# Optimization experiments

Measured on AMD Instinct MI355X. Metric: run time of the kernel, lower is better.

## Reference

```python
import jax, jax.numpy as jnp
import numpy as np

B, N, C, H, SR = 4, 4096, 512, 8, 2
HD = C // H           # head_dim = 64
SCALE = HD ** -0.5
EPS = 1e-5


def setup_inputs() -> dict:
    key = jax.random.key(0)
    ks = jax.random.split(key, 6)
    s = 0.02
    return {
        "x": jax.random.normal(ks[0], (B, N, C), jnp.float32),
        # weights stored [in, out] (transposed vs torch nn.Linear)
        "w_qkv": jax.random.normal(ks[1], (C, 3 * C), jnp.float32) * s,
        "w_proj": jax.random.normal(ks[2], (C, C), jnp.float32) * s,
        "b_proj": jnp.zeros((C,), jnp.float32),
        # depthwise conv: OIHW with I=1, feature_group_count=C
        "w_sr_conv": jax.random.normal(ks[3], (C, 1, SR, SR), jnp.float32) * s,
        "b_sr_conv": jnp.zeros((C,), jnp.float32),
        "sr_norm_scale": jnp.ones((C,), jnp.float32),
        "sr_norm_bias": jnp.zeros((C,), jnp.float32),
        "w_sr_linear": jax.random.normal(ks[4], (C, HD), jnp.float32) * s,
        "b_sr_linear": jnp.zeros((HD,), jnp.float32),
    }


def reference(x, w_qkv, w_proj, b_proj, w_sr_conv, b_sr_conv,
              sr_norm_scale, sr_norm_bias, w_sr_linear, b_sr_linear):
    Bx, Nx, Cx = x.shape
    # qkv projection (no bias), split into heads
    qkv = (x @ w_qkv).reshape(Bx, Nx, 3, H, HD).transpose(2, 0, 3, 1, 4)  # [3,B,H,N,HD]
    q, k, v = qkv[0], qkv[1], qkv[2]

    # spatial-reduction branch (sr_ratio > 1)
    S = int(Nx ** 0.5)
    x_ = x.transpose(0, 2, 1).reshape(Bx, Cx, S, S)
    x_ = jax.lax.conv_general_dilated(
        x_, w_sr_conv, window_strides=(SR, SR), padding='VALID',
        dimension_numbers=('NCHW', 'OIHW', 'NCHW'), feature_group_count=Cx)
    x_ = x_ + b_sr_conv[None, :, None, None]
    x_ = x_.reshape(Bx, Cx, -1).transpose(0, 2, 1)  # [B, M, C], M = (S/SR)^2
    # LayerNorm over C
    mu = jnp.mean(x_, axis=-1, keepdims=True)
    var = jnp.var(x_, axis=-1, keepdims=True)
    x_ = (x_ - mu) * jax.lax.rsqrt(var + EPS) * sr_norm_scale + sr_norm_bias
    x_ = x_ @ w_sr_linear + b_sr_linear  # [B, M, HD]

    # K/V compression: softmax-weighted pooling of k and v by x_ scores
    scores_k = jax.nn.softmax(jnp.einsum('bmd,bhnd->bhmn', x_, k), axis=-1)
    k = jnp.einsum('bhmn,bhnd->bhmd', scores_k, k)  # [B,H,M,HD]
    scores_v = jax.nn.softmax(jnp.einsum('bmd,bhnd->bhmn', x_, v), axis=-1)
    v = jnp.einsum('bhmn,bhnd->bhmd', scores_v, v)  # [B,H,M,HD]

    # standard attention against compressed K/V
    attn = jax.nn.softmax(jnp.einsum('bhnd,bhmd->bhnm', q, k) * SCALE, axis=-1)
    out = jnp.einsum('bhnm,bhmd->bhnd', attn, v)        # [B,H,N,HD]
    out = out.transpose(0, 2, 1, 3).reshape(Bx, Nx, Cx)  # [B,N,C]
    return out @ w_proj + b_proj
```

## Files before the change

### kernel.cpp

```cpp
#include <hip/hip_runtime.h>

typedef float f32x4 __attribute__((ext_vector_type(4)));
typedef short bf16x8 __attribute__((ext_vector_type(8)));
typedef _Float16 f16x8 __attribute__((ext_vector_type(8)));
typedef __fp16 fp16x2 __attribute__((ext_vector_type(2)));

constexpr int kB  = 4;
constexpr int kN  = 4096;
constexpr int kC  = 512;
constexpr int kH  = 8;
constexpr int kHD = 64;
constexpr int kM  = 1024;
constexpr int kC3 = 1536;

__device__ inline unsigned pkh(float a, float b) {
    union { fp16x2 h; unsigned u; } u;
    u.h = __builtin_amdgcn_cvt_pkrtz(a, b);
    return u.u;
}

__device__ inline float fdot2a(unsigned ph, unsigned ones, float acc) {
    asm("v_dot2_f32_f16 %0, %1, %2, %0" : "+v"(acc) : "v"(ph), "v"(ones));
    return acc;
}

__device__ inline void swap32p(unsigned &a, unsigned &b) {
#if __has_builtin(__builtin_amdgcn_permlane32_swap)
    auto r = __builtin_amdgcn_permlane32_swap(a, b, false, false);
    a = r[0]; b = r[1];
#else
    asm volatile("v_permlane32_swap_b32 %0, %1" : "+v"(a), "+v"(b));
#endif
}
__device__ inline void swap16p(unsigned &a, unsigned &b) {
#if __has_builtin(__builtin_amdgcn_permlane16_swap)
    auto r = __builtin_amdgcn_permlane16_swap(a, b, false, false);
    a = r[0]; b = r[1];
#else
    asm volatile("v_permlane16_swap_b32 %0, %1" : "+v"(a), "+v"(b));
#endif
}

__global__ __launch_bounds__(256) void cvt_f16(
    const float* __restrict__ X, _Float16* __restrict__ Y, int n4)
{
    int i = blockIdx.x * 256 + threadIdx.x;
    if (i >= n4) return;
    float4 v = ((const float4*)X)[i];
    union { _Float16 h[4]; short4 s; } u;
    u.h[0] = (_Float16)v.x; u.h[1] = (_Float16)v.y;
    u.h[2] = (_Float16)v.z; u.h[3] = (_Float16)v.w;
    ((short4*)Y)[i] = u.s;
}

__global__ __launch_bounds__(256) void wcvtT16(
    const float* __restrict__ W, int K, int N, _Float16* __restrict__ T16)
{
    __shared__ float T[64][65];
    const int n0 = blockIdx.x * 64, k0 = blockIdx.y * 64;
    const int t = threadIdx.x;
#pragma unroll
    for (int i = 0; i < 4; i++) {
        int c = t + i * 256;
        int row = c >> 4, col4 = (c & 15) * 4;
        *(float4*)&T[row][col4] = *(const float4*)&W[(size_t)(k0 + row) * N + n0 + col4];
    }
    __syncthreads();
#pragma unroll
    for (int i = 0; i < 4; i++) {
        int c = t + i * 256;
        int nrow = c >> 4, kc4 = (c & 15) * 4;
        union { _Float16 h[4]; short4 s; } u;
        u.h[0] = (_Float16)T[kc4 + 0][nrow];
        u.h[1] = (_Float16)T[kc4 + 1][nrow];
        u.h[2] = (_Float16)T[kc4 + 2][nrow];
        u.h[3] = (_Float16)T[kc4 + 3][nrow];
        *(short4*)&T16[(size_t)(n0 + nrow) * K + k0 + kc4] = u.s;
    }
}

__global__ __launch_bounds__(256) void transpose_hd(
    const short* __restrict__ s0, const short* __restrict__ s1,
    short* __restrict__ d0, short* __restrict__ d1, int nTok)
{
    __shared__ short T[64][72];
    const short* src = blockIdx.z == 0 ? s0 : s1;
    short*       dst = blockIdx.z == 0 ? d0 : d1;
    const int n0 = blockIdx.x * 64, bh = blockIdx.y;
    const int t = threadIdx.x;
#pragma unroll
    for (int i = 0; i < 2; i++) {
        int c = t + i * 256;
        int row = c >> 3, j = (c & 7) * 8;
        *(bf16x8*)&T[row][j] = *(const bf16x8*)&src[((size_t)bh * nTok + n0 + row) * 64 + j];
    }
    __syncthreads();
#pragma unroll
    for (int i = 0; i < 2; i++) {
        int c = t + i * 256;
        int drow = c >> 3, j = (c & 7) * 8;
        bf16x8 v;
#pragma unroll
        for (int q = 0; q < 8; q++) v[q] = T[j + q][drow];
        *(bf16x8*)&dst[((size_t)bh * 64 + drow) * nTok + n0 + j] = v;
    }
}

__global__ __launch_bounds__(256) void gemm_f16(
    const _Float16* __restrict__ A, const _Float16* __restrict__ B,
    int Md, int Nd, int Kd, int mode, float qscale,
    const float* __restrict__ bias, float* __restrict__ Cf,
    _Float16* __restrict__ q, _Float16* __restrict__ k, _Float16* __restrict__ v)
{
    __shared__ _Float16 Ash[128][40], Bsh[128][40];
    const int t = threadIdx.x, lane = t & 63, L = lane & 15, quad = lane >> 4;
    const int wave = t >> 6, wm = wave >> 1, wn = wave & 1;
    const int bm = blockIdx.y * 128, bn = blockIdx.x * 128;

    f32x4 acc[4][4];
#pragma unroll
    for (int i = 0; i < 4; i++)
#pragma unroll
        for (int j = 0; j < 4; j++) acc[i][j] = (f32x4){0.f, 0.f, 0.f, 0.f};

    for (int k0 = 0; k0 < Kd; k0 += 32) {
#pragma unroll
        for (int i = 0; i < 2; i++) {
            int c = t + i * 256;
            int row = c >> 2, j = (c & 3) * 8;
            *(f16x8*)&Ash[row][j] = *(const f16x8*)&A[(size_t)(bm + row) * Kd + k0 + j];
            *(f16x8*)&Bsh[row][j] = *(const f16x8*)&B[(size_t)(bn + row) * Kd + k0 + j];
        }
        __syncthreads();
        f16x8 af[4];
#pragma unroll
        for (int mi = 0; mi < 4; mi++)
            af[mi] = *(const f16x8*)&Ash[wm * 64 + mi * 16 + L][quad * 8];
#pragma unroll
        for (int ni = 0; ni < 4; ni++) {
            f16x8 bf = *(const f16x8*)&Bsh[wn * 64 + ni * 16 + L][quad * 8];
#pragma unroll
            for (int mi = 0; mi < 4; mi++)
                acc[mi][ni] = __builtin_amdgcn_mfma_f32_16x16x32_f16(af[mi], bf, acc[mi][ni], 0, 0, 0);
        }
        __syncthreads();
    }

    if (mode == 0) {
#pragma unroll
        for (int ni = 0; ni < 4; ni++) {
            int col = bn + wn * 64 + ni * 16 + L;
            float bb = bias ? bias[col] : 0.f;
#pragma unroll
            for (int mi = 0; mi < 4; mi++)
#pragma unroll
                for (int r = 0; r < 4; r++) {
                    int row = bm + wm * 64 + mi * 16 + quad * 4 + r;
                    Cf[(size_t)row * Nd + col] = acc[mi][ni][r] + bb;
                }
        }
    } else {
#pragma unroll
        for (int ni = 0; ni < 4; ni++) {
            int col = bn + wn * 64 + ni * 16 + L;
            int s = col >> 9, h = (col >> 6) & 7, d = col & 63;
            _Float16* dst = s == 0 ? q : s == 1 ? k : v;
            float sc = (s == 0) ? qscale : 1.0f;
#pragma unroll
            for (int mi = 0; mi < 4; mi++)
#pragma unroll
                for (int r = 0; r < 4; r++) {
                    int row = bm + wm * 64 + mi * 16 + quad * 4 + r;
                    int b = row >> 12, n = row & 4095;
                    size_t idx = (((size_t)b * 8 + h) * 4096 + n) * 64 + d;
                    dst[idx] = (_Float16)(acc[mi][ni][r] * sc);
                }
        }
    }
}

__global__ __launch_bounds__(256) void sr_fused(
    const float* __restrict__ x, const float* __restrict__ wconv,
    const float* __restrict__ bconv, const float* __restrict__ gamma,
    const float* __restrict__ beta, const float* __restrict__ wlin,
    const float* __restrict__ blin, _Float16* __restrict__ xsr)
{
    __shared__ float nbuf[512];
    __shared__ float red[8];
    __shared__ float stats[2];
    __shared__ float pbuf[4][64];

    const int m = blockIdx.x, b = blockIdx.y;
    const int oy = m >> 5, ox = m & 31;
    const int t = threadIdx.x;
    const float* xb = x + (size_t)b * kN * kC;

    float vals[2], s = 0.f, sq = 0.f;
#pragma unroll
    for (int i = 0; i < 2; i++) {
        int c = t + i * 256;
        float acc = bconv[c];
#pragma unroll
        for (int dy = 0; dy < 2; dy++)
#pragma unroll
            for (int dx = 0; dx < 2; dx++) {
                int n = (oy * 2 + dy) * 64 + (ox * 2 + dx);
                acc += xb[(size_t)n * kC + c] * wconv[c * 4 + dy * 2 + dx];
            }
        vals[i] = acc;
        s += acc; sq += acc * acc;
    }
#pragma unroll
    for (int off = 32; off > 0; off >>= 1) {
        s  += __shfl_down(s,  off);
        sq += __shfl_down(sq, off);
    }
    if ((t & 63) == 0) { red[t >> 6] = s; red[4 + (t >> 6)] = sq; }
    __syncthreads();
    if (t == 0) {
        float ts = red[0] + red[1] + red[2] + red[3];
        float tq = red[4] + red[5] + red[6] + red[7];
        float mean = ts * (1.f / 512.f);
        float var  = tq * (1.f / 512.f) - mean * mean;
        stats[0] = mean;
        stats[1] = rsqrtf(var + 1e-5f);
    }
    __syncthreads();
    const float mean = stats[0], rstd = stats[1];
#pragma unroll
    for (int i = 0; i < 2; i++) {
        int c = t + i * 256;
        nbuf[c] = (vals[i] - mean) * rstd * gamma[c] + beta[c];
    }
    __syncthreads();
    const int d = t & 63, part = t >> 6;
    float p = 0.f;
    for (int c = part * 128; c < (part + 1) * 128; c++)
        p += nbuf[c] * wlin[c * 64 + d];
    pbuf[part][d] = p;
    __syncthreads();
    if (t < 64) {
        float o = pbuf[0][t] + pbuf[1][t] + pbuf[2][t] + pbuf[3][t] + blin[t];
        xsr[((size_t)b * kM + m) * kHD + t] = (_Float16)(o * 1.44269504089f);
    }
}

__global__ __launch_bounds__(256, 4) void flash_mfma(
    const _Float16* __restrict__ Q, long q_bs, long q_hs,
    const _Float16* __restrict__ K0, const _Float16* __restrict__ K1,
    long k_bs, long k_hs,
    const _Float16* __restrict__ VT0, const _Float16* __restrict__ VT1,
    long v_bs, long v_hs, int v_rs,
    _Float16* __restrict__ O,
    long o_bs, long o_hs, long o_rs, int o_cs,
    int nKtot, int nChunks, int kvMerge,
    float* __restrict__ Opart, float* __restrict__ MLpart)
{
    __shared__ _Float16 Ks[2][64][72];
    __shared__ _Float16 VTs[2][64][72];
    const int t = threadIdx.x, lane = t & 63, L = lane & 15, quad = lane >> 4;
    const int wave = t >> 6;
    const int h = blockIdx.x & 7;
    const int rest = (blockIdx.x >> 3) + (gridDim.x >> 3) * blockIdx.y;
    int b, which, nB;
    if (kvMerge) { b = blockIdx.z >> 1; which = blockIdx.z & 1; nB = gridDim.z >> 1; }
    else         { b = blockIdx.z;      which = 0;              nB = gridDim.z; }
    const int nMblk = gridDim.x / nChunks;
    const int mblk = rest / nChunks, chunk = rest % nChunks;
    const int m0 = mblk * 128;
    const int nkc = nKtot / nChunks, nbeg = chunk * nkc, nend = nbeg + nkc;
    const unsigned kOnes = 0x3C003C00u;

    const _Float16* K_ = (which ? K1 : K0) + (size_t)b * k_bs + (size_t)h * k_hs;
    const _Float16* V_ = (which ? VT1 : VT0) + (size_t)b * v_bs + (size_t)h * v_hs;

    f16x8 qf[2][2];
#pragma unroll
    for (int s = 0; s < 2; s++) {
        const size_t qrow = (size_t)b * q_bs + (size_t)h * q_hs
                          + (size_t)(m0 + wave * 32 + s * 16 + L) * 64;
        qf[s][0] = *(const f16x8*)&Q[qrow + quad * 8];
        qf[s][1] = *(const f16x8*)&Q[qrow + 32 + quad * 8];
    }

    f32x4 Oacc[2][4];
#pragma unroll
    for (int s = 0; s < 2; s++)
#pragma unroll
        for (int i = 0; i < 4; i++) Oacc[s][i] = (f32x4){0.f, 0.f, 0.f, 0.f};
    float li[2] = {0.f, 0.f};

    const int sr = t >> 3, sj = (t & 7) * 8;

    {
        f16x8 a0 = *(const f16x8*)&K_[(size_t)(nbeg + sr) * 64 + sj];
        f16x8 a1 = *(const f16x8*)&K_[(size_t)(nbeg + sr + 32) * 64 + sj];
        f16x8 a2 = *(const f16x8*)&V_[(size_t)sr * v_rs + nbeg + sj];
        f16x8 a3 = *(const f16x8*)&V_[(size_t)(sr + 32) * v_rs + nbeg + sj];
        *(f16x8*)&Ks[0][sr][sj]       = a0;
        *(f16x8*)&Ks[0][sr + 32][sj]  = a1;
        *(f16x8*)&VTs[0][sr][sj]      = a2;
        *(f16x8*)&VTs[0][sr + 32][sj] = a3;
    }
    __syncthreads();

    int cur = 0;
    for (int n0 = nbeg; n0 < nend; n0 += 64) {
        int nn = (n0 + 64 < nend) ? n0 + 64 : nbeg;
        f16x8 kp0 = *(const f16x8*)&K_[(size_t)(nn + sr) * 64 + sj];
        f16x8 kp1 = *(const f16x8*)&K_[(size_t)(nn + sr + 32) * 64 + sj];
        f16x8 vp0 = *(const f16x8*)&V_[(size_t)sr * v_rs + nn + sj];
        f16x8 vp1 = *(const f16x8*)&V_[(size_t)(sr + 32) * v_rs + nn + sj];

        unsigned d0[2][4], d1[2][4];
#pragma unroll
        for (int c = 0; c < 4; c++) {
            f16x8 k0 = *(const f16x8*)&Ks[cur][c * 16 + L][quad * 8];
            f16x8 k1 = *(const f16x8*)&Ks[cur][c * 16 + L][32 + quad * 8];
#pragma unroll
            for (int s = 0; s < 2; s++) {
                f32x4 a = (f32x4){0.f, 0.f, 0.f, 0.f};
                a = __builtin_amdgcn_mfma_f32_16x16x32_f16(k0, qf[s][0], a, 0, 0, 0);
                a = __builtin_amdgcn_mfma_f32_16x16x32_f16(k1, qf[s][1], a, 0, 0, 0);
                float p0 = exp2f(a[0]);
                float p1 = exp2f(a[1]);
                float p2 = exp2f(a[2]);
                float p3 = exp2f(a[3]);
                d0[s][c] = pkh(p0, p1);
                d1[s][c] = pkh(p2, p3);
                li[s] = fdot2a(d0[s][c], kOnes, li[s]);
                li[s] = fdot2a(d1[s][c], kOnes, li[s]);
            }
        }

        f16x8 pt[2][2];
#pragma unroll
        for (int s = 0; s < 2; s++)
#pragma unroll
            for (int h2 = 0; h2 < 2; h2++) {
                unsigned a0 = d0[s][h2 * 2], b0 = d0[s][h2 * 2 + 1];
                swap32p(a0, b0); swap16p(a0, b0);
                unsigned a1 = d1[s][h2 * 2], b1 = d1[s][h2 * 2 + 1];
                swap32p(a1, b1); swap16p(a1, b1);
                union { unsigned u[4]; f16x8 v; } U;
                U.u[0] = a0; U.u[1] = a1; U.u[2] = b0; U.u[3] = b1;
                pt[s][h2] = U.v;
            }

#pragma unroll
        for (int h2 = 0; h2 < 2; h2++) {
#pragma unroll
            for (int dch = 0; dch < 4; dch++) {
                f16x8 vt = *(const f16x8*)&VTs[cur][dch * 16 + L][h2 * 32 + quad * 8];
                Oacc[0][dch] = __builtin_amdgcn_mfma_f32_16x16x32_f16(vt, pt[0][h2], Oacc[0][dch], 0, 0, 0);
                Oacc[1][dch] = __builtin_amdgcn_mfma_f32_16x16x32_f16(vt, pt[1][h2], Oacc[1][dch], 0, 0, 0);
            }
        }

        *(f16x8*)&Ks[cur ^ 1][sr][sj]       = kp0;
        *(f16x8*)&Ks[cur ^ 1][sr + 32][sj]  = kp1;
        *(f16x8*)&VTs[cur ^ 1][sr][sj]      = vp0;
        *(f16x8*)&VTs[cur ^ 1][sr + 32][sj] = vp1;
        __syncthreads();
        cur ^= 1;
    }

    float lt[2];
#pragma unroll
    for (int s = 0; s < 2; s++) {
        float v = li[s];
        v += __shfl_xor(v, 16);
        v += __shfl_xor(v, 32);
        lt[s] = v;
    }

    if (Opart) {
        int pid = (((which * nB + b) * gridDim.y + h) * nMblk + mblk) * nChunks + chunk;
        float* Ob = Opart + (size_t)pid * (128 * 64);
        float* Mb = MLpart + (size_t)pid * 256;
#pragma unroll
        for (int s = 0; s < 2; s++) {
            int mloc = wave * 32 + s * 16 + L;
#pragma unroll
            for (int dch = 0; dch < 4; dch++)
                *(f32x4*)&Ob[mloc * 64 + dch * 16 + quad * 4] = Oacc[s][dch];
            if (quad == 0) { Mb[mloc] = 0.f; Mb[128 + mloc] = lt[s]; }
        }
    } else {
#pragma unroll
        for (int s = 0; s < 2; s++) {
            float inv = 1.f / lt[s];
            size_t base = (size_t)b * o_bs + (size_t)h * o_hs
                        + (size_t)(m0 + wave * 32 + s * 16 + L) * o_rs;
#pragma unroll
            for (int dch = 0; dch < 4; dch++)
#pragma unroll
                for (int r = 0; r < 4; r++) {
                    int d = dch * 16 + quad * 4 + r;
                    O[base + (size_t)d * o_cs] = (_Float16)(Oacc[s][dch][r] * inv);
                }
        }
    }
}

__global__ __launch_bounds__(256) void flash_combine(
    const float* __restrict__ Opart, const float* __restrict__ MLpart,
    int nMblk, int nChunks, float cl2,
    _Float16* __restrict__ O, long o_bs, long o_hs, long o_rs, int o_cs)
{
    const int t = threadIdx.x;
    const int b = blockIdx.z, h = blockIdx.y;
    const int qm = blockIdx.x * 4 + (t >> 6), d = t & 63;
    const int mblk = qm >> 7, qloc = qm & 127;
    const int pb = ((b * gridDim.y + h) * nMblk + mblk) * nChunks;
    float mf = -INFINITY;
    for (int c = 0; c < nChunks; c++)
        mf = fmaxf(mf, MLpart[(size_t)(pb + c) * 256 + qloc]);
    float num = 0.f, den = 0.f;
    for (int c = 0; c < nChunks; c++) {
        float mc = MLpart[(size_t)(pb + c) * 256 + qloc];
        float lc = MLpart[(size_t)(pb + c) * 256 + 128 + qloc];
        float w = exp2f((mc - mf) * cl2);
        den += lc * w;
        num += Opart[(size_t)(pb + c) * 8192 + qloc * 64 + d] * w;
    }
    size_t addr = (size_t)b * o_bs + (size_t)h * o_hs + (size_t)qm * o_rs + (size_t)d * o_cs;
    O[addr] = (_Float16)(num / den);
}

extern "C" void kernel_launch(void* const* d_in, const int* in_sizes, int n_in,
                              void* d_out, int out_size, void* d_ws, size_t ws_size,
                              hipStream_t stream)
{
    const float* x      = (const float*)d_in[0];
    const float* w_qkv  = (const float*)d_in[1];
    const float* w_proj = (const float*)d_in[2];
    const float* b_proj = (const float*)d_in[3];
    const float* w_conv = (const float*)d_in[4];
    const float* b_conv = (const float*)d_in[5];
    const float* g_ln   = (const float*)d_in[6];
    const float* b_ln   = (const float*)d_in[7];
    const float* w_lin  = (const float*)d_in[8];
    const float* b_lin  = (const float*)d_in[9];
    float* out = (float*)d_out;
    (void)in_sizes; (void)n_in; (void)out_size; (void)ws_size;

    short* p = (short*)d_ws;
    size_t off = 0;
    auto alloc = [&](size_t n) { short* r = p + off; off += n; return r; };

    const size_t TN = (size_t)kB * kH * kN * kHD;
    const size_t TM = (size_t)kB * kH * kM * kHD;

    _Float16* xf16 = (_Float16*)alloc((size_t)kB * kN * kC);
    _Float16* ao   = xf16;

    _Float16* wq16 = (_Float16*)alloc((size_t)kC3 * kC);
    _Float16* wp16 = (_Float16*)alloc((size_t)kC * kC);
    _Float16* qh  = (_Float16*)alloc(TN);
    _Float16* kh  = (_Float16*)alloc(TN);
    _Float16* vh  = (_Float16*)alloc(TN);
    _Float16* kT  = (_Float16*)alloc(TN);
    _Float16* vT  = (_Float16*)alloc(TN);
    _Float16* xsr = (_Float16*)alloc((size_t)kB * kM * kHD);
    _Float16* kc  = (_Float16*)alloc(TM);
    _Float16* vc  = (_Float16*)alloc(TM);
    _Float16* vcT = (_Float16*)alloc(TM);
    float* MLpart = (float*)alloc((size_t)2048 * 256 * 2);
    float* Opart  = (float*)alloc((size_t)2048 * 8192 * 2);

    const int NCH = 4;

    cvt_f16<<<(kB * kN * kC / 4 + 255) / 256, 256, 0, stream>>>(
        x, xf16, kB * kN * kC / 4);

    wcvtT16<<<dim3(kC3 / 64, kC / 64), 256, 0, stream>>>(w_qkv, kC, kC3, wq16);
    wcvtT16<<<dim3(kC / 64, kC / 64), 256, 0, stream>>>(w_proj, kC, kC, wp16);

    gemm_f16<<<dim3(kC3 / 128, kB * kN / 128), 256, 0, stream>>>(
        xf16, wq16, kB * kN, kC3, kC, 1, 0.18033688f, nullptr, nullptr,
        qh, kh, vh);

    transpose_hd<<<dim3(kN / 64, kB * kH, 2), 256, 0, stream>>>(
        (const short*)kh, (const short*)vh, (short*)kT, (short*)vT, kN);

    sr_fused<<<dim3(kM, kB), 256, 0, stream>>>(
        x, w_conv, b_conv, g_ln, b_ln, w_lin, b_lin, xsr);

    flash_mfma<<<dim3(8 * NCH, kH, kB * 2), 256, 0, stream>>>(
        xsr, (long)kM * kHD, 0L,
        kh, vh, (long)kH * kN * kHD, (long)kN * kHD,
        kT, vT, (long)kH * kHD * kN, (long)kHD * kN, kN,
        nullptr, 0L, 0L, 0L, 0,
        kN, NCH, 1, Opart, MLpart);
    flash_combine<<<dim3(kM / 4, kH, kB), 256, 0, stream>>>(
        Opart, MLpart, 8, NCH, 1.44269504089f,
        kc, (long)kH * kM * kHD, (long)kM * kHD, 64L, 1);
    flash_combine<<<dim3(kM / 4, kH, kB), 256, 0, stream>>>(
        Opart + (size_t)1024 * 8192, MLpart + (size_t)1024 * 256, 8, NCH,
        1.44269504089f,
        vc, (long)kH * kM * kHD, (long)kM * kHD, 64L, 1);
    transpose_hd<<<dim3(kM / 64, kB * kH, 1), 256, 0, stream>>>(
        (const short*)vc, (const short*)vc, (short*)vcT, (short*)vcT, kM);

    flash_mfma<<<dim3(32, kH, kB), 256, 0, stream>>>(
        qh, (long)kH * kN * kHD, (long)kN * kHD,
        kc, kc, (long)kH * kM * kHD, (long)kM * kHD,
        vcT, vcT, (long)kH * kHD * kM, (long)kHD * kM, kM,
        ao, (long)kN * kC, 64L, (long)kC, 1,
        kM, 1, 0, nullptr, nullptr);

    gemm_f16<<<dim3(kC / 128, kB * kN / 128), 256, 0, stream>>>(
        ao, wp16, kB * kN, kC, kC, 0, 1.0f, b_proj, out,
        nullptr, nullptr, nullptr);
}
```

Measured before the change: 409.1 us.

## Load K/V fragments directly from global memory instead of LDS double buffer

The flash attention kernel no longer stages K and V^T tiles through a double-buffered shared-memory array. Each wave now loads its MFMA operand fragments straight from global memory (relying on L1/L2 caching, since all four waves read the same tiles). This drops the LDS writes and reads and the full __syncthreads, keeping only a bare s_barrier. In exchange every wave issues redundant global loads, and the software prefetch that overlapped the next tile's load with compute is lost.

```diff
diff --git a/kernel.cpp b/kernel.cpp
--- a/kernel.cpp
+++ b/kernel.cpp
@@ -256,8 +256,6 @@
     int nKtot, int nChunks, int kvMerge,
     float* __restrict__ Opart, float* __restrict__ MLpart)
 {
-    __shared__ _Float16 Ks[2][64][72];
-    __shared__ _Float16 VTs[2][64][72];
     const int t = threadIdx.x, lane = t & 63, L = lane & 15, quad = lane >> 4;
     const int wave = t >> 6;
     const int h = blockIdx.x & 7;
@@ -274,6 +272,9 @@
     const _Float16* K_ = (which ? K1 : K0) + (size_t)b * k_bs + (size_t)h * k_hs;
     const _Float16* V_ = (which ? VT1 : VT0) + (size_t)b * v_bs + (size_t)h * v_hs;
 
+    const _Float16* Krow = K_ + (size_t)L * 64 + quad * 8;
+    const _Float16* Vrow = V_ + (size_t)L * v_rs + quad * 8;
+
     f16x8 qf[2][2];
 #pragma unroll
     for (int s = 0; s < 2; s++) {
@@ -290,38 +291,23 @@
         for (int i = 0; i < 4; i++) Oacc[s][i] = (f32x4){0.f, 0.f, 0.f, 0.f};
     float li[2] = {0.f, 0.f};
 
-    const int sr = t >> 3, sj = (t & 7) * 8;
-
-    {
-        f16x8 a0 = *(const f16x8*)&K_[(size_t)(nbeg + sr) * 64 + sj];
-        f16x8 a1 = *(const f16x8*)&K_[(size_t)(nbeg + sr + 32) * 64 + sj];
-        f16x8 a2 = *(const f16x8*)&V_[(size_t)sr * v_rs + nbeg + sj];
-        f16x8 a3 = *(const f16x8*)&V_[(size_t)(sr + 32) * v_rs + nbeg + sj];
-        *(f16x8*)&Ks[0][sr][sj]       = a0;
-        *(f16x8*)&Ks[0][sr + 32][sj]  = a1;
-        *(f16x8*)&VTs[0][sr][sj]      = a2;
-        *(f16x8*)&VTs[0][sr + 32][sj] = a3;
-    }
-    __syncthreads();
-
-    int cur = 0;
     for (int n0 = nbeg; n0 < nend; n0 += 64) {
-        int nn = (n0 + 64 < nend) ? n0 + 64 : nbeg;
-        f16x8 kp0 = *(const f16x8*)&K_[(size_t)(nn + sr) * 64 + sj];
-        f16x8 kp1 = *(const f16x8*)&K_[(size_t)(nn + sr + 32) * 64 + sj];
-        f16x8 vp0 = *(const f16x8*)&V_[(size_t)sr * v_rs + nn + sj];
-        f16x8 vp1 = *(const f16x8*)&V_[(size_t)(sr + 32) * v_rs + nn + sj];
+        f16x8 kf0[4], kf1[4];
+#pragma unroll
+        for (int c = 0; c < 4; c++) {
+            const _Float16* kr = Krow + (size_t)(n0 + c * 16) * 64;
+            kf0[c] = *(const f16x8*)kr;
+            kf1[c] = *(const f16x8*)(kr + 32);
+        }
 
         unsigned d0[2][4], d1[2][4];
 #pragma unroll
         for (int c = 0; c < 4; c++) {
-            f16x8 k0 = *(const f16x8*)&Ks[cur][c * 16 + L][quad * 8];
-            f16x8 k1 = *(const f16x8*)&Ks[cur][c * 16 + L][32 + quad * 8];
 #pragma unroll
             for (int s = 0; s < 2; s++) {
                 f32x4 a = (f32x4){0.f, 0.f, 0.f, 0.f};
-                a = __builtin_amdgcn_mfma_f32_16x16x32_f16(k0, qf[s][0], a, 0, 0, 0);
-                a = __builtin_amdgcn_mfma_f32_16x16x32_f16(k1, qf[s][1], a, 0, 0, 0);
+                a = __builtin_amdgcn_mfma_f32_16x16x32_f16(kf0[c], qf[s][0], a, 0, 0, 0);
+                a = __builtin_amdgcn_mfma_f32_16x16x32_f16(kf1[c], qf[s][1], a, 0, 0, 0);
                 float p0 = exp2f(a[0]);
                 float p1 = exp2f(a[1]);
                 float p2 = exp2f(a[2]);
@@ -333,6 +319,14 @@
             }
         }
 
+        f16x8 vf[2][4];
+#pragma unroll
+        for (int h2 = 0; h2 < 2; h2++)
+#pragma unroll
+            for (int dch = 0; dch < 4; dch++)
+                vf[h2][dch] = *(const f16x8*)(Vrow + (size_t)(dch * 16) * v_rs
+                                              + n0 + h2 * 32);
+
         f16x8 pt[2][2];
 #pragma unroll
         for (int s = 0; s < 2; s++)
@@ -351,18 +345,12 @@
         for (int h2 = 0; h2 < 2; h2++) {
 #pragma unroll
             for (int dch = 0; dch < 4; dch++) {
-                f16x8 vt = *(const f16x8*)&VTs[cur][dch * 16 + L][h2 * 32 + quad * 8];
-                Oacc[0][dch] = __builtin_amdgcn_mfma_f32_16x16x32_f16(vt, pt[0][h2], Oacc[0][dch], 0, 0, 0);
-                Oacc[1][dch] = __builtin_amdgcn_mfma_f32_16x16x32_f16(vt, pt[1][h2], Oacc[1][dch], 0, 0, 0);
+                Oacc[0][dch] = __builtin_amdgcn_mfma_f32_16x16x32_f16(vf[h2][dch], pt[0][h2], Oacc[0][dch], 0, 0, 0);
+                Oacc[1][dch] = __builtin_amdgcn_mfma_f32_16x16x32_f16(vf[h2][dch], pt[1][h2], Oacc[1][dch], 0, 0, 0);
             }
         }
 
-        *(f16x8*)&Ks[cur ^ 1][sr][sj]       = kp0;
-        *(f16x8*)&Ks[cur ^ 1][sr + 32][sj]  = kp1;
-        *(f16x8*)&VTs[cur ^ 1][sr][sj]      = vp0;
-        *(f16x8*)&VTs[cur ^ 1][sr + 32][sj] = vp1;
-        __syncthreads();
-        cur ^= 1;
+        __builtin_amdgcn_s_barrier();
     }
 
     float lt[2];
```

After: 612.1 us. 49.6% more time.

## Use direct global-to-LDS loads in GEMM and store flash partials in fp16

Applied to the files above, without the earlier changes.

The GEMM tile loads now use global_load_lds to write straight into unpadded shared memory, skipping the round trip through registers. The split-K flash partial outputs are normalized and stored as fp16 with only the row sums kept. The combine step then becomes a sum weighted by those row sums, with no max pass, which roughly halves partial-buffer traffic. The trade-offs are possible LDS bank conflicts from removing the padding and slightly lower precision in the stored partials. The simplified combine relies on the max already being zero, which the old code also assumed (it wrote 0 for the max).

```diff
diff --git a/kernel.cpp b/kernel.cpp
--- a/kernel.cpp
+++ b/kernel.cpp
@@ -39,6 +39,12 @@
 #else
     asm volatile("v_permlane16_swap_b32 %0, %1" : "+v"(a), "+v"(b));
 #endif
+}
+
+__device__ inline void gl_lds16(const _Float16* g, _Float16* l) {
+    __builtin_amdgcn_global_load_lds(
+        (const __attribute__((address_space(1))) unsigned int*)(const void*)g,
+        (__attribute__((address_space(3))) unsigned int*)(void*)l, 16, 0, 0);
 }
 
 __global__ __launch_bounds__(256) void cvt_f16(
@@ -112,10 +118,11 @@
     const float* __restrict__ bias, float* __restrict__ Cf,
     _Float16* __restrict__ q, _Float16* __restrict__ k, _Float16* __restrict__ v)
 {
-    __shared__ _Float16 Ash[128][40], Bsh[128][40];
+    __shared__ _Float16 Ash[128][32], Bsh[128][32];
     const int t = threadIdx.x, lane = t & 63, L = lane & 15, quad = lane >> 4;
     const int wave = t >> 6, wm = wave >> 1, wn = wave & 1;
     const int bm = blockIdx.y * 128, bn = blockIdx.x * 128;
+    const int r16 = lane >> 2, c16 = lane & 3;
 
     f32x4 acc[4][4];
 #pragma unroll
@@ -126,10 +133,10 @@
     for (int k0 = 0; k0 < Kd; k0 += 32) {
 #pragma unroll
         for (int i = 0; i < 2; i++) {
-            int c = t + i * 256;
-            int row = c >> 2, j = (c & 3) * 8;
-            *(f16x8*)&Ash[row][j] = *(const f16x8*)&A[(size_t)(bm + row) * Kd + k0 + j];
-            *(f16x8*)&Bsh[row][j] = *(const f16x8*)&B[(size_t)(bn + row) * Kd + k0 + j];
+            int chunk = wave * 2 + i;
+            int row = chunk * 16 + r16;
+            gl_lds16(&A[(size_t)(bm + row) * Kd + k0 + c16 * 8], &Ash[chunk * 16][0]);
+            gl_lds16(&B[(size_t)(bn + row) * Kd + k0 + c16 * 8], &Bsh[chunk * 16][0]);
         }
         __syncthreads();
         f16x8 af[4];
@@ -254,7 +261,7 @@
     _Float16* __restrict__ O,
     long o_bs, long o_hs, long o_rs, int o_cs,
     int nKtot, int nChunks, int kvMerge,
-    float* __restrict__ Opart, float* __restrict__ MLpart)
+    _Float16* __restrict__ Opart, float* __restrict__ MLpart)
 {
     __shared__ _Float16 Ks[2][64][72];
     __shared__ _Float16 VTs[2][64][72];
@@ -376,15 +383,21 @@
 
     if (Opart) {
         int pid = (((which * nB + b) * gridDim.y + h) * nMblk + mblk) * nChunks + chunk;
-        float* Ob = Opart + (size_t)pid * (128 * 64);
-        float* Mb = MLpart + (size_t)pid * 256;
+        _Float16* Ob = Opart + (size_t)pid * (128 * 64);
+        float* Mb = MLpart + (size_t)pid * 128;
 #pragma unroll
         for (int s = 0; s < 2; s++) {
             int mloc = wave * 32 + s * 16 + L;
-#pragma unroll
-            for (int dch = 0; dch < 4; dch++)
-                *(f32x4*)&Ob[mloc * 64 + dch * 16 + quad * 4] = Oacc[s][dch];
-            if (quad == 0) { Mb[mloc] = 0.f; Mb[128 + mloc] = lt[s]; }
+            float inv = 1.f / lt[s];
+#pragma unroll
+            for (int dch = 0; dch < 4; dch++) {
+                union { _Float16 h[4]; uint2 u; } U;
+#pragma unroll
+                for (int r = 0; r < 4; r++)
+                    U.h[r] = (_Float16)(Oacc[s][dch][r] * inv);
+                *(uint2*)&Ob[mloc * 64 + dch * 16 + quad * 4] = U.u;
+            }
+            if (quad == 0) Mb[mloc] = lt[s];
         }
     } else {
 #pragma unroll
@@ -404,8 +417,8 @@
 }
 
 __global__ __launch_bounds__(256) void flash_combine(
-    const float* __restrict__ Opart, const float* __restrict__ MLpart,
-    int nMblk, int nChunks, float cl2,
+    const _Float16* __restrict__ Opart, const float* __restrict__ MLpart,
+    int nMblk, int nChunks,
     _Float16* __restrict__ O, long o_bs, long o_hs, long o_rs, int o_cs)
 {
     const int t = threadIdx.x;
@@ -413,16 +426,11 @@
     const int qm = blockIdx.x * 4 + (t >> 6), d = t & 63;
     const int mblk = qm >> 7, qloc = qm & 127;
     const int pb = ((b * gridDim.y + h) * nMblk + mblk) * nChunks;
-    float mf = -INFINITY;
-    for (int c = 0; c < nChunks; c++)
-        mf = fmaxf(mf, MLpart[(size_t)(pb + c) * 256 + qloc]);
     float num = 0.f, den = 0.f;
     for (int c = 0; c < nChunks; c++) {
-        float mc = MLpart[(size_t)(pb + c) * 256 + qloc];
-        float lc = MLpart[(size_t)(pb + c) * 256 + 128 + qloc];
-        float w = exp2f((mc - mf) * cl2);
-        den += lc * w;
-        num += Opart[(size_t)(pb + c) * 8192 + qloc * 64 + d] * w;
+        float lc = MLpart[(size_t)(pb + c) * 128 + qloc];
+        num += lc * (float)Opart[(size_t)(pb + c) * 8192 + qloc * 64 + d];
+        den += lc;
     }
     size_t addr = (size_t)b * o_bs + (size_t)h * o_hs + (size_t)qm * o_rs + (size_t)d * o_cs;
     O[addr] = (_Float16)(num / den);
@@ -466,8 +474,8 @@
     _Float16* kc  = (_Float16*)alloc(TM);
     _Float16* vc  = (_Float16*)alloc(TM);
     _Float16* vcT = (_Float16*)alloc(TM);
-    float* MLpart = (float*)alloc((size_t)2048 * 256 * 2);
-    float* Opart  = (float*)alloc((size_t)2048 * 8192 * 2);
+    float*    MLpart = (float*)alloc((size_t)2048 * 128 * 2);
+    _Float16* Opart  = (_Float16*)alloc((size_t)2048 * 8192);
 
     const int NCH = 4;
 
@@ -494,11 +502,10 @@
         nullptr, 0L, 0L, 0L, 0,
         kN, NCH, 1, Opart, MLpart);
     flash_combine<<<dim3(kM / 4, kH, kB), 256, 0, stream>>>(
-        Opart, MLpart, 8, NCH, 1.44269504089f,
+        Opart, MLpart, 8, NCH,
         kc, (long)kH * kM * kHD, (long)kM * kHD, 64L, 1);
     flash_combine<<<dim3(kM / 4, kH, kB), 256, 0, stream>>>(
-        Opart + (size_t)1024 * 8192, MLpart + (size_t)1024 * 256, 8, NCH,
-        1.44269504089f,
+        Opart + (size_t)1024 * 8192, MLpart + (size_t)1024 * 128, 8, NCH,
         vc, (long)kH * kM * kHD, (long)kM * kHD, 64L, 1);
     transpose_hd<<<dim3(kM / 64, kB * kH, 1), 256, 0, stream>>>(
         (const short*)vc, (const short*)vc, (short*)vcT, (short*)vcT, kM);
```

Result: faster. 394.9 us (-3.5%).
